# Kernel tuning notes

Measured on AMD Instinct MI355X. Metric: run time of the kernel, lower is better.

The kernel has to match this reference:

```python
import jax, jax.numpy as jnp
import numpy as np

N, E, D = 50000, 400000, 512
EPS = 1e-5


def setup_inputs() -> dict:
    key = jax.random.key(0)
    ks = jax.random.split(key, 5)
    scale = 1.0 / np.sqrt(D)
    x = jax.random.normal(ks[0], (N, D), dtype=jnp.float32)
    edge_index = jax.random.randint(ks[1], (2, E), 0, N, dtype=jnp.int32)
    W_l = jax.random.normal(ks[2], (D, D), dtype=jnp.float32) * scale
    b_l = jnp.zeros((D,), dtype=jnp.float32)
    W_r = jax.random.normal(ks[3], (D, D), dtype=jnp.float32) * scale
    gamma = jnp.ones((D,), dtype=jnp.float32)
    beta = jnp.zeros((D,), dtype=jnp.float32)
    return {"x": x, "edge_index": edge_index, "W_l": W_l, "b_l": b_l,
            "W_r": W_r, "gamma": gamma, "beta": beta}


def reference(x, edge_index, W_l, b_l, W_r, gamma, beta):
    n = x.shape[0]
    src, dst = edge_index[0], edge_index[1]
    # SAGEConv mean aggregation: mean of source features over incoming edges
    agg = jax.ops.segment_sum(x[src], dst, num_segments=n)           # [N, D]
    cnt = jax.ops.segment_sum(jnp.ones((src.shape[0],), x.dtype), dst,
                              num_segments=n)                         # [N]
    mean_agg = agg / jnp.maximum(cnt, 1.0)[:, None]
    # out = lin_l(mean_agg) + lin_r(x)  (PyG SAGEConv: bias on lin_l only)
    h = mean_agg @ W_l.T + b_l + x @ W_r.T
    # BatchNorm over node dimension (training-mode batch stats)
    mu = jnp.mean(h, axis=0)
    var = jnp.var(h, axis=0)
    h = (h - mu) * jax.lax.rsqrt(var + EPS) * gamma + beta
    # relu + residual (input_dim == output_dim -> identity residual);
    # dropout is identity in eval mode
    return jax.nn.relu(h) + x
```

## Files before the change

kernel.cpp:

```cpp
#include <hip/hip_runtime.h>

#define NNODES 50000
#define NEDGES 400000
#define DIM    512
#define SCAN_BLOCKS 196

typedef float f32x4 __attribute__((ext_vector_type(4)));
typedef __bf16 bf16x8 __attribute__((ext_vector_type(8)));


__device__ __forceinline__ unsigned bf16_rne_bits(float f) {
  unsigned u = __float_as_uint(f);
  return u + 0x7FFF + ((u >> 16) & 1);
}

__device__ __forceinline__ void async16(void* lds, const void* g) {
  __builtin_amdgcn_global_load_lds(
      (const __attribute__((address_space(1))) unsigned*)g,
      (__attribute__((address_space(3))) unsigned*)lds, 16, 0, 0);
}


__global__ void count_kernel(const int* __restrict__ dst, int* __restrict__ cnt) {
  int i = blockIdx.x * blockDim.x + threadIdx.x;
  if (i < NEDGES) atomicAdd(&cnt[dst[i]], 1);
}

__global__ void scan1_kernel(const int* __restrict__ cnt, int* __restrict__ part,
                             int* __restrict__ bsum) {
  __shared__ int ws4[4];
  int i = blockIdx.x * 256 + (int)threadIdx.x;
  int lane = threadIdx.x & 63, wid = threadIdx.x >> 6;
  int v = (i < NNODES) ? cnt[i] : 0;
  int s = v;
  #pragma unroll
  for (int d = 1; d < 64; d <<= 1) { int t = __shfl_up(s, d); if (lane >= d) s += t; }
  if (lane == 63) ws4[wid] = s;
  __syncthreads();
  int pre = 0;
  #pragma unroll
  for (int k = 0; k < 4; ++k) if (k < wid) pre += ws4[k];
  if (i < NNODES) part[i] = pre + s - v;
  if (threadIdx.x == 255) bsum[blockIdx.x] = pre + s;
}

__global__ void scan2_kernel(const int* __restrict__ bsum, int* __restrict__ boff) {
  __shared__ int ws4[4];
  int lane = threadIdx.x & 63, wid = threadIdx.x >> 6;
  int i = (int)threadIdx.x;
  int v = (i < SCAN_BLOCKS) ? bsum[i] : 0;
  int s = v;
  #pragma unroll
  for (int d = 1; d < 64; d <<= 1) { int t = __shfl_up(s, d); if (lane >= d) s += t; }
  if (lane == 63) ws4[wid] = s;
  __syncthreads();
  int pre = 0;
  #pragma unroll
  for (int k = 0; k < 4; ++k) if (k < wid) pre += ws4[k];
  if (i < SCAN_BLOCKS) boff[i] = pre + s - v;
}

__global__ void scan3_kernel(int* __restrict__ offs, const int* __restrict__ boff,
                             int* __restrict__ cursor) {
  int i = blockIdx.x * 256 + (int)threadIdx.x;
  if (i < NNODES) {
    int o = offs[i] + boff[blockIdx.x];
    offs[i] = o;
    cursor[i] = o;
  }
}

__global__ void fill_kernel(const int* __restrict__ src, const int* __restrict__ dst,
                            int* __restrict__ cursor, int* __restrict__ csr) {
  int i = blockIdx.x * blockDim.x + threadIdx.x;
  if (i < NEDGES) {
    int d = dst[i];
    int p = atomicAdd(&cursor[d], 1);
    csr[p] = src[i];
  }
}


__global__ void convert_x_kernel(const float* __restrict__ x,
                                 unsigned short* __restrict__ xhi) {
  int t = blockIdx.x * 256 + (int)threadIdx.x;
  const float* s = x + (size_t)t * 8;
  float f[8];
  *(float4*)&f[0] = ((const float4*)s)[0];
  *(float4*)&f[4] = ((const float4*)s)[1];
  uint4 p;
  unsigned h0 = bf16_rne_bits(f[0]), h1 = bf16_rne_bits(f[1]);
  unsigned h2 = bf16_rne_bits(f[2]), h3 = bf16_rne_bits(f[3]);
  unsigned h4 = bf16_rne_bits(f[4]), h5 = bf16_rne_bits(f[5]);
  unsigned h6 = bf16_rne_bits(f[6]), h7 = bf16_rne_bits(f[7]);
  p.x = (h0 >> 16) | (h1 & 0xFFFF0000u);
  p.y = (h2 >> 16) | (h3 & 0xFFFF0000u);
  p.z = (h4 >> 16) | (h5 & 0xFFFF0000u);
  p.w = (h6 >> 16) | (h7 & 0xFFFF0000u);
  *(uint4*)(xhi + (size_t)t * 8) = p;
}


__global__ void aggregate_kernel(const unsigned short* __restrict__ xhi,
                                 const int* __restrict__ offs,
                                 const int* __restrict__ cnt, const int* __restrict__ csr,
                                 unsigned short* __restrict__ ahi,
                                 unsigned short* __restrict__ alo) {
  int node = blockIdx.x * 4 + (int)(threadIdx.x >> 6);
  int lane = threadIdx.x & 63;
  if (node >= NNODES) return;
  int off = offs[node];
  int deg = cnt[node];
  float a[8] = {0.f, 0.f, 0.f, 0.f, 0.f, 0.f, 0.f, 0.f};
  for (int i = 0; i < deg; ++i) {
    int s = csr[off + i];
    uint4 v = *(const uint4*)(xhi + (size_t)s * DIM + lane * 8);
    a[0] += __uint_as_float(v.x << 16);
    a[1] += __uint_as_float(v.x & 0xFFFF0000u);
    a[2] += __uint_as_float(v.y << 16);
    a[3] += __uint_as_float(v.y & 0xFFFF0000u);
    a[4] += __uint_as_float(v.z << 16);
    a[5] += __uint_as_float(v.z & 0xFFFF0000u);
    a[6] += __uint_as_float(v.w << 16);
    a[7] += __uint_as_float(v.w & 0xFFFF0000u);
  }
  float w = 1.0f / fmaxf((float)deg, 1.0f);
  unsigned hb[8], lb[8];
  #pragma unroll
  for (int j = 0; j < 8; ++j) {
    float m = a[j] * w;
    unsigned r = bf16_rne_bits(m);
    hb[j] = r;
    lb[j] = bf16_rne_bits(m - __uint_as_float(r & 0xFFFF0000u));
  }
  uint4 ph, pl;
  ph.x = (hb[0] >> 16) | (hb[1] & 0xFFFF0000u);
  ph.y = (hb[2] >> 16) | (hb[3] & 0xFFFF0000u);
  ph.z = (hb[4] >> 16) | (hb[5] & 0xFFFF0000u);
  ph.w = (hb[6] >> 16) | (hb[7] & 0xFFFF0000u);
  pl.x = (lb[0] >> 16) | (lb[1] & 0xFFFF0000u);
  pl.y = (lb[2] >> 16) | (lb[3] & 0xFFFF0000u);
  pl.z = (lb[4] >> 16) | (lb[5] & 0xFFFF0000u);
  pl.w = (lb[6] >> 16) | (lb[7] & 0xFFFF0000u);
  *(uint4*)(ahi + (size_t)node * DIM + lane * 8) = ph;
  *(uint4*)(alo + (size_t)node * DIM + lane * 8) = pl;
}


__global__ void convert_w_kernel(const float* __restrict__ Wl, const float* __restrict__ Wr,
                                 unsigned short* __restrict__ bhi,
                                 unsigned short* __restrict__ blo) {
  int t = blockIdx.x * blockDim.x + threadIdx.x;
  int n  = t >> 7;
  int k  = (t & 127) * 8;
  const float* s = (k < 512) ? (Wl + (size_t)n * 512 + k)
                             : (Wr + (size_t)n * 512 + (k - 512));
  float f[8];
  *(float4*)&f[0] = ((const float4*)s)[0];
  *(float4*)&f[4] = ((const float4*)s)[1];
  unsigned hi[8], lo[8];
  #pragma unroll
  for (int i = 0; i < 8; ++i) {
    unsigned r = bf16_rne_bits(f[i]);
    hi[i] = r;
    lo[i] = bf16_rne_bits(f[i] - __uint_as_float(r & 0xFFFF0000u));
  }
  uint4 ph, pl;
  ph.x = (hi[0] >> 16) | (hi[1] & 0xFFFF0000u);
  ph.y = (hi[2] >> 16) | (hi[3] & 0xFFFF0000u);
  ph.z = (hi[4] >> 16) | (hi[5] & 0xFFFF0000u);
  ph.w = (hi[6] >> 16) | (hi[7] & 0xFFFF0000u);
  pl.x = (lo[0] >> 16) | (lo[1] & 0xFFFF0000u);
  pl.y = (lo[2] >> 16) | (lo[3] & 0xFFFF0000u);
  pl.z = (lo[4] >> 16) | (lo[5] & 0xFFFF0000u);
  pl.w = (lo[6] >> 16) | (lo[7] & 0xFFFF0000u);
  *(uint4*)(bhi + (size_t)n * 1024 + k) = ph;
  *(uint4*)(blo + (size_t)n * 1024 + k) = pl;
}


__launch_bounds__(256, 2)
__global__ void mfma_gemm(const unsigned short* __restrict__ AggHi,
                          const unsigned short* __restrict__ AggLo,
                          const float* __restrict__ X,
                          const unsigned short* __restrict__ Bhi,
                          const unsigned short* __restrict__ Blo,
                          float* __restrict__ H,
                          float* __restrict__ sums, float* __restrict__ sqs) {
  __shared__ char lds[65536];
  char* As_hi = lds;
  char* As_lo = lds + 16384;
  char* Bs_hi = lds + 32768;
  char* Bs_lo = lds + 49152;

  const int tid  = (int)threadIdx.x;
  const int lane = tid & 63;
  const int w    = tid >> 6;

  const int g    = (int)blockIdx.x;
  const int prow = ((g >> 5) << 3) + (g & 7);
  const int cblk = (g >> 3) & 3;
  const int colBase = cblk * 128;
  const int rowBase = prow * 128;

  const int q  = lane >> 4;
  const int r2 = lane & 15;
  const int wr = w >> 1, wc = w & 1;

  const int schunk = (((tid & 7) ^ ((tid >> 3) & 7)) << 4);
  const int srowq  = tid >> 3;

  f32x4 zero = {0.f, 0.f, 0.f, 0.f};
  f32x4 acc[4][4];
  #pragma unroll
  for (int i = 0; i < 4; ++i)
    #pragma unroll
    for (int j = 0; j < 4; ++j) acc[i][j] = zero;

  for (int t = 0; t < 16; ++t) {
    const int kk = t * 64;

    #pragma unroll
    for (int c = 0; c < 4; ++c) {
      int row = c * 32 + srowq;
      const char* gh = (const char*)Bhi + (size_t)(colBase + row) * 2048 + kk * 2 + schunk;
      const char* gl = (const char*)Blo + (size_t)(colBase + row) * 2048 + kk * 2 + schunk;
      async16(Bs_hi + c * 4096 + w * 1024, gh);
      async16(Bs_lo + c * 4096 + w * 1024, gl);
    }

    if (t < 8) {
      #pragma unroll
      for (int c = 0; c < 4; ++c) {
        int row = c * 32 + srowq;
        int gr = rowBase + row;
        if (gr >= NNODES) gr = NNODES - 1;
        const char* gh = (const char*)AggHi + (size_t)gr * 1024 + kk * 2 + schunk;
        const char* gl = (const char*)AggLo + (size_t)gr * 1024 + kk * 2 + schunk;
        async16(As_hi + c * 4096 + w * 1024, gh);
        async16(As_lo + c * 4096 + w * 1024, gl);
      }
    } else {
      const int kf = kk - 512;
      float4 av[8];
      #pragma unroll
      for (int c = 0; c < 8; ++c) {
        int idx16 = c * 256 + tid;
        int row   = idx16 >> 4;
        int col16 = idx16 & 15;
        int gr = rowBase + row;
        if (gr >= NNODES) gr = NNODES - 1;
        av[c] = *(const float4*)(X + (size_t)gr * 512 + kf + col16 * 4);
      }
      #pragma unroll
      for (int c = 0; c < 8; ++c) {
        int idx16 = c * 256 + tid;
        int row   = idx16 >> 4;
        int col16 = idx16 & 15;
        int off = row * 128 + ((col16 * 8) ^ ((row & 7) << 4));
        float f0 = av[c].x, f1 = av[c].y, f2 = av[c].z, f3 = av[c].w;
        unsigned r0 = bf16_rne_bits(f0), r1 = bf16_rne_bits(f1);
        unsigned r2b = bf16_rne_bits(f2), r3 = bf16_rne_bits(f3);
        float l0 = f0 - __uint_as_float(r0 & 0xFFFF0000u);
        float l1 = f1 - __uint_as_float(r1 & 0xFFFF0000u);
        float l2 = f2 - __uint_as_float(r2b & 0xFFFF0000u);
        float l3 = f3 - __uint_as_float(r3 & 0xFFFF0000u);
        uint2 hw, lw;
        hw.x = (r0 >> 16) | (r1 & 0xFFFF0000u);
        hw.y = (r2b >> 16) | (r3 & 0xFFFF0000u);
        lw.x = (bf16_rne_bits(l0) >> 16) | (bf16_rne_bits(l1) & 0xFFFF0000u);
        lw.y = (bf16_rne_bits(l2) >> 16) | (bf16_rne_bits(l3) & 0xFFFF0000u);
        *(uint2*)(As_hi + off) = hw;
        *(uint2*)(As_lo + off) = lw;
      }
    }

    __syncthreads();

    #pragma unroll
    for (int ks = 0; ks < 2; ++ks) {
      const int cOff = (((ks * 4 + q) ^ (r2 & 7)) << 4);
      bf16x8 ah[4], al[4], bh[4], bl[4];
      #pragma unroll
      for (int i = 0; i < 4; ++i) {
        int arow = wr * 64 + i * 16 + r2;
        ah[i] = *(const bf16x8*)(As_hi + arow * 128 + cOff);
        al[i] = *(const bf16x8*)(As_lo + arow * 128 + cOff);
        int brow = wc * 64 + i * 16 + r2;
        bh[i] = *(const bf16x8*)(Bs_hi + brow * 128 + cOff);
        bl[i] = *(const bf16x8*)(Bs_lo + brow * 128 + cOff);
      }
      #pragma unroll
      for (int i = 0; i < 4; ++i)
        #pragma unroll
        for (int j = 0; j < 4; ++j) {
          acc[i][j] = __builtin_amdgcn_mfma_f32_16x16x32_bf16(al[i], bh[j], acc[i][j], 0, 0, 0);
          acc[i][j] = __builtin_amdgcn_mfma_f32_16x16x32_bf16(ah[i], bl[j], acc[i][j], 0, 0, 0);
          acc[i][j] = __builtin_amdgcn_mfma_f32_16x16x32_bf16(ah[i], bh[j], acc[i][j], 0, 0, 0);
        }
    }
    __syncthreads();
  }

  #pragma unroll
  for (int i = 0; i < 4; ++i) {
    #pragma unroll
    for (int r = 0; r < 4; ++r) {
      int gm = rowBase + wr * 64 + i * 16 + q * 4 + r;
      if (gm < NNODES) {
        float* hp = H + (size_t)gm * 512 + colBase + wc * 64 + r2;
        #pragma unroll
        for (int j = 0; j < 4; ++j) hp[j * 16] = acc[i][j][r];
      }
    }
  }

  float* lsum = (float*)lds;
  float* lsq  = (float*)(lds + 512);
  if (tid < 128) lsum[tid] = 0.f;
  else if (tid < 256) lsq[tid - 128] = 0.f;
  __syncthreads();
  #pragma unroll
  for (int j = 0; j < 4; ++j) {
    float p = 0.f, qs = 0.f;
    #pragma unroll
    for (int i = 0; i < 4; ++i)
      #pragma unroll
      for (int r = 0; r < 4; ++r) {
        int gm = rowBase + wr * 64 + i * 16 + q * 4 + r;
        if (gm < NNODES) {
          float v = acc[i][j][r];
          p += v;
          qs += v * v;
        }
      }
    int cl = wc * 64 + j * 16 + r2;
    atomicAdd(&lsum[cl], p);
    atomicAdd(&lsq[cl], qs);
  }
  __syncthreads();
  if (tid < 128) atomicAdd(&sums[colBase + tid], lsum[tid]);
  else if (tid < 256) atomicAdd(&sqs[colBase + tid - 128], lsq[tid - 128]);
}


__global__ void bn_final(const float* __restrict__ sums, const float* __restrict__ sqs,
                         const float* __restrict__ gamma, const float* __restrict__ beta,
                         float* __restrict__ scale, float* __restrict__ shift) {
  int c = threadIdx.x;
  float mu  = sums[c] * (1.0f / (float)NNODES);
  float var = sqs[c] * (1.0f / (float)NNODES) - mu * mu;
  float inv = rsqrtf(var + 1e-5f);
  float sc = inv * gamma[c];
  scale[c] = sc;
  shift[c] = beta[c] - mu * sc;
}

__global__ void bn_apply(float* __restrict__ H, const float* __restrict__ X,
                         const float* __restrict__ scale, const float* __restrict__ shift) {
  const size_t total = (size_t)NNODES * (DIM / 4);
  for (size_t i = (size_t)blockIdx.x * blockDim.x + threadIdx.x; i < total;
       i += (size_t)gridDim.x * blockDim.x) {
    int c4 = ((int)(i & (DIM / 4 - 1))) * 4;
    float4 h = ((const float4*)H)[i];
    float4 xv = ((const float4*)X)[i];
    float4 r;
    r.x = fmaxf(fmaf(h.x, scale[c4 + 0], shift[c4 + 0]), 0.f) + xv.x;
    r.y = fmaxf(fmaf(h.y, scale[c4 + 1], shift[c4 + 1]), 0.f) + xv.y;
    r.z = fmaxf(fmaf(h.z, scale[c4 + 2], shift[c4 + 2]), 0.f) + xv.z;
    r.w = fmaxf(fmaf(h.w, scale[c4 + 3], shift[c4 + 3]), 0.f) + xv.w;
    ((float4*)H)[i] = r;
  }
}


extern "C" void kernel_launch(void* const* d_in, const int* in_sizes, int n_in,
                              void* d_out, int out_size, void* d_ws, size_t ws_size,
                              hipStream_t stream) {
  (void)in_sizes; (void)n_in; (void)out_size; (void)ws_size;
  const float* x     = (const float*)d_in[0];
  const int*   ei    = (const int*)d_in[1];
  const float* Wl    = (const float*)d_in[2];
  const float* Wr    = (const float*)d_in[4];
  const float* gamma = (const float*)d_in[5];
  const float* beta  = (const float*)d_in[6];
  float* H = (float*)d_out;

  const int* src = ei;
  const int* dst = ei + NEDGES;

  unsigned short* xhi = (unsigned short*)d_out;

  char* w = (char*)d_ws;
  unsigned short* ahi = (unsigned short*)w;  w += (size_t)NNODES * DIM * 2;
  unsigned short* alo = (unsigned short*)w;  w += (size_t)NNODES * DIM * 2;
  unsigned short* bhi = (unsigned short*)w;  w += (size_t)512 * 1024 * 2;
  unsigned short* blo = (unsigned short*)w;  w += (size_t)512 * 1024 * 2;
  int* cnt    = (int*)w;              w += (size_t)NNODES * 4;
  int* offs   = (int*)w;              w += (size_t)NNODES * 4;
  int* cursor = (int*)w;              w += (size_t)NNODES * 4;
  int* csr    = (int*)w;              w += (size_t)NEDGES * 4;
  int* bsum   = (int*)w;              w += (size_t)256 * 4;
  int* boff   = (int*)w;              w += (size_t)256 * 4;
  float* sums = (float*)w;            w += (size_t)DIM * 4;
  float* sqs  = (float*)w;            w += (size_t)DIM * 4;
  float* scale= (float*)w;            w += (size_t)DIM * 4;
  float* shift= (float*)w;            w += (size_t)DIM * 4;

  hipMemsetAsync(cnt, 0, (size_t)NNODES * 4, stream);
  hipMemsetAsync(sums, 0, (size_t)2 * DIM * 4, stream);

  count_kernel<<<(NEDGES + 255) / 256, 256, 0, stream>>>(dst, cnt);
  scan1_kernel<<<SCAN_BLOCKS, 256, 0, stream>>>(cnt, offs, bsum);
  scan2_kernel<<<1, 256, 0, stream>>>(bsum, boff);
  scan3_kernel<<<SCAN_BLOCKS, 256, 0, stream>>>(offs, boff, cursor);
  fill_kernel<<<(NEDGES + 255) / 256, 256, 0, stream>>>(src, dst, cursor, csr);
  convert_w_kernel<<<256, 256, 0, stream>>>(Wl, Wr, bhi, blo);
  convert_x_kernel<<<(NNODES * DIM / 8 + 255) / 256, 256, 0, stream>>>(x, xhi);
  aggregate_kernel<<<(NNODES + 3) / 4, 256, 0, stream>>>(xhi, offs, cnt, csr, ahi, alo);
  mfma_gemm<<<1568, 256, 0, stream>>>(ahi, alo, x, bhi, blo, H, sums, sqs);
  bn_final<<<1, DIM, 0, stream>>>(sums, sqs, gamma, beta, scale, shift);
  bn_apply<<<2048, 256, 0, stream>>>(H, x, scale, shift);
}
```

Before: 532.6 us.

## Replace split-bf16 three-pass GEMM with single-pass fp16 MFMA

Converts x, the aggregated means and the weights to plain fp16 instead of bf16 hi/lo pairs, and runs one fp16 MFMA per tile instead of three bf16 MFMAs. The GEMM now streams the fp16 copy of x through async LDS loads instead of converting fp32 x in-kernel. LDS drops to 32 KB and launch bounds allow 4 blocks per CU. This cuts MFMA work, LDS traffic and aggregate/convert write bandwidth, at the cost of fp16 precision (about 11 bits of mantissa) in place of the emulated near-fp32 accuracy, which may matter against the tolerance.

```diff
diff --git a/kernel.cpp b/kernel.cpp
--- a/kernel.cpp
+++ b/kernel.cpp
@@ -6,13 +6,8 @@
 #define SCAN_BLOCKS 196
 
 typedef float f32x4 __attribute__((ext_vector_type(4)));
-typedef __bf16 bf16x8 __attribute__((ext_vector_type(8)));
-
-
-__device__ __forceinline__ unsigned bf16_rne_bits(float f) {
-  unsigned u = __float_as_uint(f);
-  return u + 0x7FFF + ((u >> 16) & 1);
-}
+typedef _Float16 f16x8 __attribute__((ext_vector_type(8)));
+
 
 __device__ __forceinline__ void async16(void* lds, const void* g) {
   __builtin_amdgcn_global_load_lds(
@@ -81,31 +76,23 @@
 }
 
 
-__global__ void convert_x_kernel(const float* __restrict__ x,
-                                 unsigned short* __restrict__ xhi) {
+__global__ void convert_x_kernel(const float* __restrict__ x, _Float16* __restrict__ xp) {
   int t = blockIdx.x * 256 + (int)threadIdx.x;
-  const float* s = x + (size_t)t * 8;
-  float f[8];
-  *(float4*)&f[0] = ((const float4*)s)[0];
-  *(float4*)&f[4] = ((const float4*)s)[1];
-  uint4 p;
-  unsigned h0 = bf16_rne_bits(f[0]), h1 = bf16_rne_bits(f[1]);
-  unsigned h2 = bf16_rne_bits(f[2]), h3 = bf16_rne_bits(f[3]);
-  unsigned h4 = bf16_rne_bits(f[4]), h5 = bf16_rne_bits(f[5]);
-  unsigned h6 = bf16_rne_bits(f[6]), h7 = bf16_rne_bits(f[7]);
-  p.x = (h0 >> 16) | (h1 & 0xFFFF0000u);
-  p.y = (h2 >> 16) | (h3 & 0xFFFF0000u);
-  p.z = (h4 >> 16) | (h5 & 0xFFFF0000u);
-  p.w = (h6 >> 16) | (h7 & 0xFFFF0000u);
-  *(uint4*)(xhi + (size_t)t * 8) = p;
-}
-
-
-__global__ void aggregate_kernel(const unsigned short* __restrict__ xhi,
+  const float4* s = (const float4*)(x + (size_t)t * 8);
+  float4 f0 = s[0], f1 = s[1];
+  f16x8 o;
+  o[0] = (_Float16)f0.x; o[1] = (_Float16)f0.y;
+  o[2] = (_Float16)f0.z; o[3] = (_Float16)f0.w;
+  o[4] = (_Float16)f1.x; o[5] = (_Float16)f1.y;
+  o[6] = (_Float16)f1.z; o[7] = (_Float16)f1.w;
+  *(f16x8*)(xp + (size_t)t * 8) = o;
+}
+
+
+__global__ void aggregate_kernel(const _Float16* __restrict__ xp,
                                  const int* __restrict__ offs,
                                  const int* __restrict__ cnt, const int* __restrict__ csr,
-                                 unsigned short* __restrict__ ahi,
-                                 unsigned short* __restrict__ alo) {
+                                 _Float16* __restrict__ agg) {
   int node = blockIdx.x * 4 + (int)(threadIdx.x >> 6);
   int lane = threadIdx.x & 63;
   if (node >= NNODES) return;
@@ -114,42 +101,20 @@
   float a[8] = {0.f, 0.f, 0.f, 0.f, 0.f, 0.f, 0.f, 0.f};
   for (int i = 0; i < deg; ++i) {
     int s = csr[off + i];
-    uint4 v = *(const uint4*)(xhi + (size_t)s * DIM + lane * 8);
-    a[0] += __uint_as_float(v.x << 16);
-    a[1] += __uint_as_float(v.x & 0xFFFF0000u);
-    a[2] += __uint_as_float(v.y << 16);
-    a[3] += __uint_as_float(v.y & 0xFFFF0000u);
-    a[4] += __uint_as_float(v.z << 16);
-    a[5] += __uint_as_float(v.z & 0xFFFF0000u);
-    a[6] += __uint_as_float(v.w << 16);
-    a[7] += __uint_as_float(v.w & 0xFFFF0000u);
+    f16x8 v = *(const f16x8*)(xp + (size_t)s * DIM + lane * 8);
+    #pragma unroll
+    for (int j = 0; j < 8; ++j) a[j] += (float)v[j];
   }
   float w = 1.0f / fmaxf((float)deg, 1.0f);
-  unsigned hb[8], lb[8];
-  #pragma unroll
-  for (int j = 0; j < 8; ++j) {
-    float m = a[j] * w;
-    unsigned r = bf16_rne_bits(m);
-    hb[j] = r;
-    lb[j] = bf16_rne_bits(m - __uint_as_float(r & 0xFFFF0000u));
-  }
-  uint4 ph, pl;
-  ph.x = (hb[0] >> 16) | (hb[1] & 0xFFFF0000u);
-  ph.y = (hb[2] >> 16) | (hb[3] & 0xFFFF0000u);
-  ph.z = (hb[4] >> 16) | (hb[5] & 0xFFFF0000u);
-  ph.w = (hb[6] >> 16) | (hb[7] & 0xFFFF0000u);
-  pl.x = (lb[0] >> 16) | (lb[1] & 0xFFFF0000u);
-  pl.y = (lb[2] >> 16) | (lb[3] & 0xFFFF0000u);
-  pl.z = (lb[4] >> 16) | (lb[5] & 0xFFFF0000u);
-  pl.w = (lb[6] >> 16) | (lb[7] & 0xFFFF0000u);
-  *(uint4*)(ahi + (size_t)node * DIM + lane * 8) = ph;
-  *(uint4*)(alo + (size_t)node * DIM + lane * 8) = pl;
+  f16x8 o;
+  #pragma unroll
+  for (int j = 0; j < 8; ++j) o[j] = (_Float16)(a[j] * w);
+  *(f16x8*)(agg + (size_t)node * DIM + lane * 8) = o;
 }
 
 
 __global__ void convert_w_kernel(const float* __restrict__ Wl, const float* __restrict__ Wr,
-                                 unsigned short* __restrict__ bhi,
-                                 unsigned short* __restrict__ blo) {
+                                 _Float16* __restrict__ Wc) {
   int t = blockIdx.x * blockDim.x + threadIdx.x;
   int n  = t >> 7;
   int k  = (t & 127) * 8;
@@ -158,40 +123,22 @@
   float f[8];
   *(float4*)&f[0] = ((const float4*)s)[0];
   *(float4*)&f[4] = ((const float4*)s)[1];
-  unsigned hi[8], lo[8];
-  #pragma unroll
-  for (int i = 0; i < 8; ++i) {
-    unsigned r = bf16_rne_bits(f[i]);
-    hi[i] = r;
-    lo[i] = bf16_rne_bits(f[i] - __uint_as_float(r & 0xFFFF0000u));
-  }
-  uint4 ph, pl;
-  ph.x = (hi[0] >> 16) | (hi[1] & 0xFFFF0000u);
-  ph.y = (hi[2] >> 16) | (hi[3] & 0xFFFF0000u);
-  ph.z = (hi[4] >> 16) | (hi[5] & 0xFFFF0000u);
-  ph.w = (hi[6] >> 16) | (hi[7] & 0xFFFF0000u);
-  pl.x = (lo[0] >> 16) | (lo[1] & 0xFFFF0000u);
-  pl.y = (lo[2] >> 16) | (lo[3] & 0xFFFF0000u);
-  pl.z = (lo[4] >> 16) | (lo[5] & 0xFFFF0000u);
-  pl.w = (lo[6] >> 16) | (lo[7] & 0xFFFF0000u);
-  *(uint4*)(bhi + (size_t)n * 1024 + k) = ph;
-  *(uint4*)(blo + (size_t)n * 1024 + k) = pl;
-}
-
-
-__launch_bounds__(256, 2)
-__global__ void mfma_gemm(const unsigned short* __restrict__ AggHi,
-                          const unsigned short* __restrict__ AggLo,
-                          const float* __restrict__ X,
-                          const unsigned short* __restrict__ Bhi,
-                          const unsigned short* __restrict__ Blo,
+  f16x8 o;
+  #pragma unroll
+  for (int i = 0; i < 8; ++i) o[i] = (_Float16)f[i];
+  *(f16x8*)(Wc + (size_t)n * 1024 + k) = o;
+}
+
+
+__launch_bounds__(256, 4)
+__global__ void mfma_gemm(const _Float16* __restrict__ Agg,
+                          const _Float16* __restrict__ Xp,
+                          const _Float16* __restrict__ Wc,
                           float* __restrict__ H,
                           float* __restrict__ sums, float* __restrict__ sqs) {
-  __shared__ char lds[65536];
-  char* As_hi = lds;
-  char* As_lo = lds + 16384;
-  char* Bs_hi = lds + 32768;
-  char* Bs_lo = lds + 49152;
+  __shared__ char lds[32768];
+  char* As = lds;
+  char* Bs = lds + 16384;
 
   const int tid  = (int)threadIdx.x;
   const int lane = tid & 63;
@@ -218,61 +165,19 @@
     for (int j = 0; j < 4; ++j) acc[i][j] = zero;
 
   for (int t = 0; t < 16; ++t) {
-    const int kk = t * 64;
+    const _Float16* Ap = (t < 8) ? Agg : Xp;
+    const int kbA = (t & 7) * 128;
+    const int kbB = t * 128;
 
     #pragma unroll
     for (int c = 0; c < 4; ++c) {
       int row = c * 32 + srowq;
-      const char* gh = (const char*)Bhi + (size_t)(colBase + row) * 2048 + kk * 2 + schunk;
-      const char* gl = (const char*)Blo + (size_t)(colBase + row) * 2048 + kk * 2 + schunk;
-      async16(Bs_hi + c * 4096 + w * 1024, gh);
-      async16(Bs_lo + c * 4096 + w * 1024, gl);
-    }
-
-    if (t < 8) {
-      #pragma unroll
-      for (int c = 0; c < 4; ++c) {
-        int row = c * 32 + srowq;
-        int gr = rowBase + row;
-        if (gr >= NNODES) gr = NNODES - 1;
-        const char* gh = (const char*)AggHi + (size_t)gr * 1024 + kk * 2 + schunk;
-        const char* gl = (const char*)AggLo + (size_t)gr * 1024 + kk * 2 + schunk;
-        async16(As_hi + c * 4096 + w * 1024, gh);
-        async16(As_lo + c * 4096 + w * 1024, gl);
-      }
-    } else {
-      const int kf = kk - 512;
-      float4 av[8];
-      #pragma unroll
-      for (int c = 0; c < 8; ++c) {
-        int idx16 = c * 256 + tid;
-        int row   = idx16 >> 4;
-        int col16 = idx16 & 15;
-        int gr = rowBase + row;
-        if (gr >= NNODES) gr = NNODES - 1;
-        av[c] = *(const float4*)(X + (size_t)gr * 512 + kf + col16 * 4);
-      }
-      #pragma unroll
-      for (int c = 0; c < 8; ++c) {
-        int idx16 = c * 256 + tid;
-        int row   = idx16 >> 4;
-        int col16 = idx16 & 15;
-        int off = row * 128 + ((col16 * 8) ^ ((row & 7) << 4));
-        float f0 = av[c].x, f1 = av[c].y, f2 = av[c].z, f3 = av[c].w;
-        unsigned r0 = bf16_rne_bits(f0), r1 = bf16_rne_bits(f1);
-        unsigned r2b = bf16_rne_bits(f2), r3 = bf16_rne_bits(f3);
-        float l0 = f0 - __uint_as_float(r0 & 0xFFFF0000u);
-        float l1 = f1 - __uint_as_float(r1 & 0xFFFF0000u);
-        float l2 = f2 - __uint_as_float(r2b & 0xFFFF0000u);
-        float l3 = f3 - __uint_as_float(r3 & 0xFFFF0000u);
-        uint2 hw, lw;
-        hw.x = (r0 >> 16) | (r1 & 0xFFFF0000u);
-        hw.y = (r2b >> 16) | (r3 & 0xFFFF0000u);
-        lw.x = (bf16_rne_bits(l0) >> 16) | (bf16_rne_bits(l1) & 0xFFFF0000u);
-        lw.y = (bf16_rne_bits(l2) >> 16) | (bf16_rne_bits(l3) & 0xFFFF0000u);
-        *(uint2*)(As_hi + off) = hw;
-        *(uint2*)(As_lo + off) = lw;
-      }
+      const char* gb = (const char*)Wc + (size_t)(colBase + row) * 2048 + kbB + schunk;
+      async16(Bs + c * 4096 + w * 1024, gb);
+      int gr = rowBase + row;
+      if (gr >= NNODES) gr = NNODES - 1;
+      const char* ga = (const char*)Ap + (size_t)gr * 1024 + kbA + schunk;
+      async16(As + c * 4096 + w * 1024, ga);
     }
 
     __syncthreads();
@@ -280,24 +185,19 @@
     #pragma unroll
     for (int ks = 0; ks < 2; ++ks) {
       const int cOff = (((ks * 4 + q) ^ (r2 & 7)) << 4);
-      bf16x8 ah[4], al[4], bh[4], bl[4];
+      f16x8 a[4], b[4];
       #pragma unroll
       for (int i = 0; i < 4; ++i) {
         int arow = wr * 64 + i * 16 + r2;
-        ah[i] = *(const bf16x8*)(As_hi + arow * 128 + cOff);
-        al[i] = *(const bf16x8*)(As_lo + arow * 128 + cOff);
+        a[i] = *(const f16x8*)(As + arow * 128 + cOff);
         int brow = wc * 64 + i * 16 + r2;
-        bh[i] = *(const bf16x8*)(Bs_hi + brow * 128 + cOff);
-        bl[i] = *(const bf16x8*)(Bs_lo + brow * 128 + cOff);
+        b[i] = *(const f16x8*)(Bs + brow * 128 + cOff);
       }
       #pragma unroll
       for (int i = 0; i < 4; ++i)
         #pragma unroll
-        for (int j = 0; j < 4; ++j) {
-          acc[i][j] = __builtin_amdgcn_mfma_f32_16x16x32_bf16(al[i], bh[j], acc[i][j], 0, 0, 0);
-          acc[i][j] = __builtin_amdgcn_mfma_f32_16x16x32_bf16(ah[i], bl[j], acc[i][j], 0, 0, 0);
-          acc[i][j] = __builtin_amdgcn_mfma_f32_16x16x32_bf16(ah[i], bh[j], acc[i][j], 0, 0, 0);
-        }
+        for (int j = 0; j < 4; ++j)
+          acc[i][j] = __builtin_amdgcn_mfma_f32_16x16x32_f16(a[i], b[j], acc[i][j], 0, 0, 0);
     }
     __syncthreads();
   }
@@ -389,23 +289,20 @@
   const int* src = ei;
   const int* dst = ei + NEDGES;
 
-  unsigned short* xhi = (unsigned short*)d_out;
-
   char* w = (char*)d_ws;
-  unsigned short* ahi = (unsigned short*)w;  w += (size_t)NNODES * DIM * 2;
-  unsigned short* alo = (unsigned short*)w;  w += (size_t)NNODES * DIM * 2;
-  unsigned short* bhi = (unsigned short*)w;  w += (size_t)512 * 1024 * 2;
-  unsigned short* blo = (unsigned short*)w;  w += (size_t)512 * 1024 * 2;
-  int* cnt    = (int*)w;              w += (size_t)NNODES * 4;
-  int* offs   = (int*)w;              w += (size_t)NNODES * 4;
-  int* cursor = (int*)w;              w += (size_t)NNODES * 4;
-  int* csr    = (int*)w;              w += (size_t)NEDGES * 4;
-  int* bsum   = (int*)w;              w += (size_t)256 * 4;
-  int* boff   = (int*)w;              w += (size_t)256 * 4;
-  float* sums = (float*)w;            w += (size_t)DIM * 4;
-  float* sqs  = (float*)w;            w += (size_t)DIM * 4;
-  float* scale= (float*)w;            w += (size_t)DIM * 4;
-  float* shift= (float*)w;            w += (size_t)DIM * 4;
+  _Float16* xp  = (_Float16*)w;  w += (size_t)NNODES * DIM * 2;
+  _Float16* agg = (_Float16*)w;  w += (size_t)NNODES * DIM * 2;
+  _Float16* wcc = (_Float16*)w;  w += (size_t)512 * 1024 * 2;
+  int* cnt    = (int*)w;         w += (size_t)NNODES * 4;
+  int* offs   = (int*)w;         w += (size_t)NNODES * 4;
+  int* cursor = (int*)w;         w += (size_t)NNODES * 4;
+  int* csr    = (int*)w;         w += (size_t)NEDGES * 4;
+  int* bsum   = (int*)w;         w += (size_t)256 * 4;
+  int* boff   = (int*)w;         w += (size_t)256 * 4;
+  float* sums = (float*)w;       w += (size_t)DIM * 4;
+  float* sqs  = (float*)w;       w += (size_t)DIM * 4;
+  float* scale= (float*)w;       w += (size_t)DIM * 4;
+  float* shift= (float*)w;       w += (size_t)DIM * 4;
 
   hipMemsetAsync(cnt, 0, (size_t)NNODES * 4, stream);
   hipMemsetAsync(sums, 0, (size_t)2 * DIM * 4, stream);
@@ -415,10 +312,10 @@
   scan2_kernel<<<1, 256, 0, stream>>>(bsum, boff);
   scan3_kernel<<<SCAN_BLOCKS, 256, 0, stream>>>(offs, boff, cursor);
   fill_kernel<<<(NEDGES + 255) / 256, 256, 0, stream>>>(src, dst, cursor, csr);
-  convert_w_kernel<<<256, 256, 0, stream>>>(Wl, Wr, bhi, blo);
-  convert_x_kernel<<<(NNODES * DIM / 8 + 255) / 256, 256, 0, stream>>>(x, xhi);
-  aggregate_kernel<<<(NNODES + 3) / 4, 256, 0, stream>>>(xhi, offs, cnt, csr, ahi, alo);
-  mfma_gemm<<<1568, 256, 0, stream>>>(ahi, alo, x, bhi, blo, H, sums, sqs);
+  convert_w_kernel<<<256, 256, 0, stream>>>(Wl, Wr, wcc);
+  convert_x_kernel<<<(NNODES * DIM / 8 + 255) / 256, 256, 0, stream>>>(x, xp);
+  aggregate_kernel<<<(NNODES + 3) / 4, 256, 0, stream>>>(xp, offs, cnt, csr, agg);
+  mfma_gemm<<<1568, 256, 0, stream>>>(agg, xp, wcc, H, sums, sqs);
   bn_final<<<1, DIM, 0, stream>>>(sums, sqs, gamma, beta, scale, shift);
   bn_apply<<<2048, 256, 0, stream>>>(H, x, scale, shift);
 }
```

New measurement: 431.1 us. -19.1%, faster.
